# Optimization experiments

Hardware: AMD Instinct MI355X
Metric: run time of the kernel (lower is better)

Reference implementation:

```python
import jax, jax.numpy as jnp
import numpy as np
from jax import lax

B, C, FH, FW = 2, 128, 96, 160
H, W = 384, 640
NH, NP = 4, 9
T = 0.5


def conv(x, w, b, groups=1):
    pad = w.shape[2] // 2
    y = lax.conv_general_dilated(x, w, (1, 1), [(pad, pad), (pad, pad)],
                                 dimension_numbers=('NCHW', 'OIHW', 'NCHW'),
                                 feature_group_count=groups)
    return y + b[None, :, None, None]


def lrelu(x):
    return jnp.where(x >= 0, x, 0.1 * x)


def resize(x, h, w):
    # torch F.interpolate(mode='bilinear', align_corners=False, antialias=False)
    return jax.image.resize(x, (x.shape[0], x.shape[1], h, w), method='linear', antialias=False)


def grid_sample(vals, gx, gy, align_corners):
    # vals: (N, Ch, Hv, Wv); gx, gy: (N, Ho, Wo) normalized coords in [-1, 1]
    # bilinear, padding_mode='border'
    N, Ch, Hv, Wv = vals.shape
    if align_corners:
        x = (gx + 1.0) * 0.5 * (Wv - 1)
        y = (gy + 1.0) * 0.5 * (Hv - 1)
    else:
        x = ((gx + 1.0) * Wv - 1.0) * 0.5
        y = ((gy + 1.0) * Hv - 1.0) * 0.5
    x = jnp.clip(x, 0.0, Wv - 1.0)
    y = jnp.clip(y, 0.0, Hv - 1.0)
    x0 = jnp.floor(x)
    y0 = jnp.floor(y)
    wx = (x - x0)[:, None]  # (N,1,Ho,Wo)
    wy = (y - y0)[:, None]
    x0i = x0.astype(jnp.int32)
    y0i = y0.astype(jnp.int32)
    x1i = jnp.minimum(x0i + 1, Wv - 1)
    y1i = jnp.minimum(y0i + 1, Hv - 1)
    flat = vals.reshape(N, Ch, Hv * Wv)
    gather = jax.vmap(lambda v, i: jnp.take(v, i, axis=1))  # (Ch,HW),(Ho,Wo)->(Ch,Ho,Wo)
    v00 = gather(flat, y0i * Wv + x0i)
    v01 = gather(flat, y0i * Wv + x1i)
    v10 = gather(flat, y1i * Wv + x0i)
    v11 = gather(flat, y1i * Wv + x1i)
    return (v00 * (1 - wx) * (1 - wy) + v01 * wx * (1 - wy)
            + v10 * (1 - wx) * wy + v11 * wx * wy)


def warp(feat, flow):
    b, c, h, w = feat.shape
    if flow.shape[2:] != (h, w):
        sh, sw = h / flow.shape[2], w / flow.shape[3]
        flow = resize(flow, h, w) * jnp.array([sw, sh], flow.dtype)[None, :, None, None]
    gy, gx = jnp.meshgrid(jnp.arange(h, dtype=jnp.float32),
                          jnp.arange(w, dtype=jnp.float32), indexing='ij')
    gxn = 2.0 * (gx[None] + flow[:, 0]) / max(w - 1, 1) - 1.0
    gyn = 2.0 * (gy[None] + flow[:, 1]) / max(h - 1, 1) - 1.0
    return grid_sample(feat, gxn, gyn, True)


def group_norm(x, g, b, groups=8, eps=1e-5):
    B_, C_, h, w = x.shape
    xr = x.reshape(B_, groups, C_ // groups, h, w)
    m = xr.mean(axis=(2, 3, 4), keepdims=True)
    v = xr.var(axis=(2, 3, 4), keepdims=True)
    xn = ((xr - m) * lax.rsqrt(v + eps)).reshape(B_, C_, h, w)
    return xn * g[None, :, None, None] + b[None, :, None, None]


def deform_attn(q, src, ow0, ob0, ow1, ob1, aw0, ab0, aw1, ab1, vw, vb, pw, pb):
    b, c, h, w = q.shape
    hd = c // NH
    off = conv(lrelu(conv(q, ow0, ob0, groups=NH)), ow1, ob1).reshape(b, NH, NP, 2, h, w)
    attn = conv(lrelu(conv(q, aw0, ab0, groups=NH)), aw1, ab1).reshape(b, NH, NP, h, w)
    attn = jax.nn.softmax(attn, axis=2)
    vals = conv(src, vw, vb).reshape(b * NH, hd, h, w)
    gy, gx = jnp.meshgrid(jnp.arange(h, dtype=jnp.float32),
                          jnp.arange(w, dtype=jnp.float32), indexing='ij')
    sx = gx[None, None, None] + off[:, :, :, 0]  # (b,NH,NP,h,w)
    sy = gy[None, None, None] + off[:, :, :, 1]
    gxn = (2.0 * sx / max(w - 1, 1) - 1.0).reshape(b * NH, NP * h, w)
    gyn = (2.0 * sy / max(h - 1, 1) - 1.0).reshape(b * NH, NP * h, w)
    samp = grid_sample(vals, gxn, gyn, False).reshape(b, NH, hd, NP, h, w)
    out = (samp * attn[:, :, None]).sum(axis=3).reshape(b, c, h, w)
    return conv(out, pw, pb)


def setup_inputs() -> dict:
    key = jax.random.key(0)
    ks = jax.random.split(key, 24)
    rn = lambda k, s, sc: jax.random.normal(k, s, jnp.float32) * sc
    # offset conv bias: 3x3 regular grid init (n_points=9), padded with zeros
    gs = 3
    base = []
    for dy in range(gs):
        for dx in range(gs):
            base += [dx - gs // 2, dy - gs // 2]
    ob1 = np.zeros(NH * NP * 2, np.float32)
    ob1[:len(base)] = np.asarray(base, np.float32)
    return {
        'feat1': rn(ks[0], (B, C, FH, FW), 1.0),
        'feat2': rn(ks[1], (B, C, FH, FW), 1.0),
        'flow_fwd': rn(ks[2], (B, 2, H, W), 3.0),
        'flow_bwd': rn(ks[3], (B, 2, H, W), 3.0),
        'edge1': jax.random.uniform(ks[4], (B, 1, H, W), jnp.float32),
        'edge2': jax.random.uniform(ks[5], (B, 1, H, W), jnp.float32),
        'fuse_w0': rn(ks[6], (C, 2 * C + 3, 3, 3), 0.02),
        'fuse_b0': jnp.zeros((C,), jnp.float32),
        'fuse_w1': rn(ks[7], (C, C, 3, 3), 0.02),
        'fuse_b1': jnp.zeros((C,), jnp.float32),
        'gn_g': jnp.ones((C,), jnp.float32),
        'gn_b': jnp.zeros((C,), jnp.float32),
        'off_w0': rn(ks[8], (C, C // NH, 3, 3), 0.02),
        'off_b0': jnp.zeros((C,), jnp.float32),
        'off_w1': rn(ks[9], (NH * NP * 2, C, 1, 1), 0.01),
        'off_b1': jnp.asarray(ob1),
        'aw_w0': rn(ks[10], (C, C // NH, 3, 3), 0.02),
        'aw_b0': jnp.zeros((C,), jnp.float32),
        'aw_w1': rn(ks[11], (NH * NP, C, 1, 1), 0.02),
        'aw_b1': jnp.zeros((NH * NP,), jnp.float32),
        'val_w': rn(ks[12], (C, C, 1, 1), 0.05),
        'val_b': jnp.zeros((C,), jnp.float32),
        'out_w': rn(ks[13], (C, C, 1, 1), 0.05),
        'out_b': jnp.zeros((C,), jnp.float32),
        'ffn_w0': rn(ks[14], (2 * C, C, 1, 1), 0.05),
        'ffn_b0': jnp.zeros((2 * C,), jnp.float32),
        'ffn_w1': rn(ks[15], (C, 2 * C, 1, 1), 0.05),
        'ffn_b1': jnp.zeros((C,), jnp.float32),
        'dec_w0': rn(ks[16], (64, C, 3, 3), 0.03),
        'dec_b0': jnp.zeros((64,), jnp.float32),
        'dec_w1': rn(ks[17], (32, 64, 3, 3), 0.05),
        'dec_b1': jnp.zeros((32,), jnp.float32),
        'dec_w2': rn(ks[18], (3, 32, 3, 3), 0.05),
        'dec_b2': jnp.zeros((3,), jnp.float32),
    }


def reference(feat1, feat2, flow_fwd, flow_bwd, edge1, edge2,
              fuse_w0, fuse_b0, fuse_w1, fuse_b1, gn_g, gn_b,
              off_w0, off_b0, off_w1, off_b1, aw_w0, aw_b0, aw_w1, aw_b1,
              val_w, val_b, out_w, out_b, ffn_w0, ffn_b0, ffn_w1, ffn_b1,
              dec_w0, dec_b0, dec_w1, dec_b1, dec_w2, dec_b2):
    b, c, fh, fw = feat1.shape
    h, w = edge1.shape[2], edge1.shape[3]
    f1w = warp(feat1, flow_fwd * T)
    f2w = warp(feat2, flow_bwd * (1.0 - T))
    e1 = resize(edge1, fh, fw)
    e2 = resize(edge2, fh, fw)
    tmap = jnp.full((b, 1, fh, fw), T, feat1.dtype)
    fused = jnp.concatenate([f1w, f2w, e1, e2, tmap], axis=1)
    x = lrelu(conv(lrelu(conv(fused, fuse_w0, fuse_b0)), fuse_w1, fuse_b1))
    source = f1w * (1.0 - T) + f2w * T
    x = x + deform_attn(group_norm(x, gn_g, gn_b), source,
                        off_w0, off_b0, off_w1, off_b1,
                        aw_w0, aw_b0, aw_w1, aw_b1,
                        val_w, val_b, out_w, out_b)
    x = x + conv(jax.nn.gelu(conv(x, ffn_w0, ffn_b0), approximate=False), ffn_w1, ffn_b1)
    x = resize(x, h, w)
    x = lrelu(conv(x, dec_w0, dec_b0))
    x = lrelu(conv(x, dec_w1, dec_b1))
    return jax.nn.sigmoid(conv(x, dec_w2, dec_b2))
```

## Files before the change

kernel.cpp:

```cpp
#include <hip/hip_runtime.h>

typedef _Float16 f16;
typedef _Float16 f16x8 __attribute__((ext_vector_type(8)));
typedef float f32x4 __attribute__((ext_vector_type(4)));

constexpr int Bn = 2, Cn = 128, FH = 96, FW = 160, Hh = 384, Wh = 640;
constexpr int HWl = FH * FW;
constexpr int NHd = 4, NPt = 9;

#define DEVINL __device__ __forceinline__

DEVINL f32x4 zero4() { f32x4 z; z[0] = 0.f; z[1] = 0.f; z[2] = 0.f; z[3] = 0.f; return z; }
DEVINL f16x8 zero8() {
  f16x8 z;
#pragma unroll
  for (int j = 0; j < 8; ++j) z[j] = (f16)0.f;
  return z;
}

template<int ACT> DEVINL float activ(float v) {
  if (ACT == 1) return v >= 0.f ? v : 0.1f * v;
  if (ACT == 2) return 0.5f * v * (1.f + erff(v * 0.70710678118654752f));
  if (ACT == 3) return 1.f / (1.f + expf(-v));
  return v;
}

__global__ __launch_bounds__(256) void k_zero(f16* __restrict__ p, int n8)
{
  int i = blockIdx.x * 256 + threadIdx.x;
  if (i < n8) *(f16x8*)&p[(size_t)i * 8] = zero8();
}

struct PrepJob { const float* w; f16* wf; int Cout, cin_g, cout_g, KS, CoF, taps, CoFt, cf0, blk0; };
struct PrepArgs { PrepJob j[12]; };

__global__ __launch_bounds__(256) void k_wprep_all(PrepArgs a)
{
  int jb = 0;
#pragma unroll
  for (int t = 1; t < 12; ++t) if ((int)blockIdx.x >= a.j[t].blk0) jb = t;
  PrepJob J = a.j[jb];
  int idx = (blockIdx.x - J.blk0) * 256 + threadIdx.x;
  int total = J.taps * J.KS * J.CoF * 64;
  if (idx >= total) return;
  int lane = idx & 63;
  int rest = idx >> 6;
  int cf = rest % J.CoF;
  int rest2 = rest / J.CoF;
  int ks = rest2 % J.KS;
  int tap = rest2 / J.KS;
  int co = cf * 16 + (lane & 15);
  f16x8 v = zero8();
#pragma unroll
  for (int j = 0; j < 8; ++j) {
    int cip = ks * 32 + (lane >> 4) * 8 + j;
    int cil = cip - (co / J.cout_g) * J.cin_g;
    float x = 0.f;
    if (co < J.Cout && cil >= 0 && cil < J.cin_g)
      x = J.w[((size_t)co * J.cin_g + cil) * J.taps + tap];
    v[j] = (f16)x;
  }
  size_t oidx = (((size_t)tap * J.KS + ks) * J.CoFt + J.cf0 + cf) * 64 + lane;
  *(f16x8*)&J.wf[oidx * 8] = v;
}

__global__ __launch_bounds__(256) void k_tr_h(
    const float* __restrict__ feat1, const float* __restrict__ feat2,
    f16* __restrict__ t1, f16* __restrict__ t2)
{
  int idx = blockIdx.x * blockDim.x + threadIdx.x;
  if (idx >= 2 * Bn * HWl * 8) return;
  int cq = idx & 7;
  int pix = (idx >> 3) % HWl;
  int z = idx / (8 * HWl);
  int b = z & 1;
  const float* src = (z >> 1) ? feat2 : feat1;
  f16* dst = (z >> 1) ? t2 : t1;
  int c0 = cq * 16;
  f16x8 v0, v1;
#pragma unroll
  for (int j = 0; j < 8; ++j) {
    v0[j] = (f16)src[(size_t)(b * Cn + c0 + j) * HWl + pix];
    v1[j] = (f16)src[(size_t)(b * Cn + c0 + 8 + j) * HWl + pix];
  }
  f16* dp = dst + ((size_t)b * HWl + pix) * 128 + c0;
  *(f16x8*)dp = v0;
  *(f16x8*)(dp + 8) = v1;
}

__global__ __launch_bounds__(256) void k_warp_fuse_h(
    const f16* __restrict__ t1, const f16* __restrict__ t2,
    const float* __restrict__ flowf, const float* __restrict__ flowb,
    const float* __restrict__ edge1, const float* __restrict__ edge2,
    f16* __restrict__ fused, f16* __restrict__ src)
{
  int idx = blockIdx.x * blockDim.x + threadIdx.x;
  if (idx >= Bn * HWl * 8) return;
  int cq = idx & 7;
  int pix = (idx >> 3) % HWl;
  int b = idx / (8 * HWl);
  int j = pix % FW;
  int i = pix / FW;

  const int y4 = 4 * i + 1, x4 = 4 * j + 1;
  const float* p;
  p = flowf + (size_t)((b * 2 + 0) * Hh + y4) * Wh + x4;
  float fx1 = 0.03125f * (p[0] + p[1] + p[Wh] + p[Wh + 1]);
  p = flowf + (size_t)((b * 2 + 1) * Hh + y4) * Wh + x4;
  float fy1 = 0.03125f * (p[0] + p[1] + p[Wh] + p[Wh + 1]);
  p = flowb + (size_t)((b * 2 + 0) * Hh + y4) * Wh + x4;
  float fx2 = 0.03125f * (p[0] + p[1] + p[Wh] + p[Wh + 1]);
  p = flowb + (size_t)((b * 2 + 1) * Hh + y4) * Wh + x4;
  float fy2 = 0.03125f * (p[0] + p[1] + p[Wh] + p[Wh + 1]);

  float sx1 = fminf(fmaxf((float)j + fx1, 0.f), (float)(FW - 1));
  float sy1 = fminf(fmaxf((float)i + fy1, 0.f), (float)(FH - 1));
  float sx2 = fminf(fmaxf((float)j + fx2, 0.f), (float)(FW - 1));
  float sy2 = fminf(fmaxf((float)i + fy2, 0.f), (float)(FH - 1));

  int x10 = (int)floorf(sx1), y10 = (int)floorf(sy1);
  int x11 = min(x10 + 1, FW - 1), y11 = min(y10 + 1, FH - 1);
  float wx1 = sx1 - (float)x10, wy1 = sy1 - (float)y10;
  int x20 = (int)floorf(sx2), y20 = (int)floorf(sy2);
  int x21 = min(x20 + 1, FW - 1), y21 = min(y20 + 1, FH - 1);
  float wx2 = sx2 - (float)x20, wy2 = sy2 - (float)y20;

  float a00 = (1.f - wx1) * (1.f - wy1), a01 = wx1 * (1.f - wy1);
  float a10 = (1.f - wx1) * wy1,         a11 = wx1 * wy1;
  float c00 = (1.f - wx2) * (1.f - wy2), c01 = wx2 * (1.f - wy2);
  float c10 = (1.f - wx2) * wy2,         c11 = wx2 * wy2;

  int c0 = cq * 16;
  const f16* b1 = t1 + (size_t)b * HWl * 128 + c0;
  const f16* b2 = t2 + (size_t)b * HWl * 128 + c0;
  const f16x8* p100 = (const f16x8*)&b1[(size_t)(y10 * FW + x10) * 128];
  const f16x8* p101 = (const f16x8*)&b1[(size_t)(y10 * FW + x11) * 128];
  const f16x8* p110 = (const f16x8*)&b1[(size_t)(y11 * FW + x10) * 128];
  const f16x8* p111 = (const f16x8*)&b1[(size_t)(y11 * FW + x11) * 128];
  const f16x8* p200 = (const f16x8*)&b2[(size_t)(y20 * FW + x20) * 128];
  const f16x8* p201 = (const f16x8*)&b2[(size_t)(y20 * FW + x21) * 128];
  const f16x8* p210 = (const f16x8*)&b2[(size_t)(y21 * FW + x20) * 128];
  const f16x8* p211 = (const f16x8*)&b2[(size_t)(y21 * FW + x21) * 128];

  f16* fp = fused + ((size_t)b * HWl + pix) * 288;
  f16* sp = src + ((size_t)b * HWl + pix) * 128;

#pragma unroll
  for (int h = 0; h < 2; ++h) {
    f16x8 u00 = p100[h], u01 = p101[h], u10 = p110[h], u11 = p111[h];
    f16x8 w00 = p200[h], w01 = p201[h], w10 = p210[h], w11 = p211[h];
    f16x8 r1, r2, rs;
#pragma unroll
    for (int k = 0; k < 8; ++k) {
      float v1 = (float)u00[k] * a00 + (float)u01[k] * a01
               + (float)u10[k] * a10 + (float)u11[k] * a11;
      float v2 = (float)w00[k] * c00 + (float)w01[k] * c01
               + (float)w10[k] * c10 + (float)w11[k] * c11;
      r1[k] = (f16)v1; r2[k] = (f16)v2; rs[k] = (f16)(0.5f * (v1 + v2));
    }
    *(f16x8*)(fp + c0 + h * 8) = r1;
    *(f16x8*)(fp + 128 + c0 + h * 8) = r2;
    *(f16x8*)(sp + c0 + h * 8) = rs;
  }

  if (cq == 0) {
    p = edge1 + (size_t)(b * Hh + y4) * Wh + x4;
    float e1v = 0.25f * (p[0] + p[1] + p[Wh] + p[Wh + 1]);
    p = edge2 + (size_t)(b * Hh + y4) * Wh + x4;
    float e2v = 0.25f * (p[0] + p[1] + p[Wh] + p[Wh + 1]);
    fp[256] = (f16)e1v;
    fp[257] = (f16)e2v;
    fp[258] = (f16)0.5f;
#pragma unroll
    for (int c = 259; c < 288; ++c) fp[c] = (f16)0.f;
  }
}

template<int ACT, int M, int NF, int W, int KS>
__global__ __launch_bounds__(256, 2) void k_conv3g(
    const f16* __restrict__ X, const f16* __restrict__ Wf,
    const float* __restrict__ bias, const float* __restrict__ bias2, int bsplit,
    f16* __restrict__ Out, const f16* __restrict__ zpage,
    int CoF, int Cs_in, int Cs_out, int Htot,
    int in_r0, int in_rows, int out_r0, int out_rows,
    int ogr0, int nrows, int coTiles)
{
  int wid = blockIdx.x * 4 + (threadIdx.x >> 6);
  int lane = threadIdx.x & 63;
  int l15 = lane & 15, l4 = lane >> 4;
  int pixTiles = nrows * W / (M * 16);
  if (wid >= pixTiles * coTiles) return;
  int coT = wid % coTiles;
  int pixT = wid / coTiles;
  int b = blockIdx.z;
  int base = pixT * (M * 16);
  int row = ogr0 + base / W;
  int colB = base % W;

  f32x4 acc[M][NF];
#pragma unroll
  for (int mf = 0; mf < M; ++mf)
#pragma unroll
    for (int nf = 0; nf < NF; ++nf) acc[mf][nf] = zero4();

  const f16* rp[3];
#pragma unroll
  for (int ky = 0; ky < 3; ++ky) {
    int srow = row + ky - 1;
    bool rv = (srow >= 0 && srow < Htot);
    int crow = min(max(srow, in_r0), in_r0 + in_rows - 1);
    const f16* real = X + ((size_t)(b * in_rows + (crow - in_r0)) * W) * Cs_in + l4 * 8;
    rp[ky] = rv ? real : (zpage + l4 * 8);
  }
  int sc[3][M]; bool okc[3][M];
#pragma unroll
  for (int kx = 0; kx < 3; ++kx)
#pragma unroll
    for (int mf = 0; mf < M; ++mf) {
      int scol = colB + mf * 16 + l15 + kx - 1;
      okc[kx][mf] = (unsigned)scol < (unsigned)W;
      sc[kx][mf] = min(max(scol, 0), W - 1);
    }

  const f16* wb = Wf + (size_t)coT * NF * 512;
  constexpr int G = KS * 3;
  constexpr int NLD = 3 * (M + NF);
  constexpr int NMM = 3 * M * NF;

  f16x8 Afb[2][3][M];
  f16x8 Bfb[2][3][NF];

  auto loadGroup = [&](int g, int buf) {
    int cs = g / 3, ky = g % 3;
#pragma unroll
    for (int kx = 0; kx < 3; ++kx) {
#pragma unroll
      for (int mf = 0; mf < M; ++mf) {
        f16x8 t = *(const f16x8*)&rp[ky][(size_t)sc[kx][mf] * Cs_in + cs * 32];
        if ((kx == 0 && mf == 0) || (kx == 2 && mf == M - 1))
          t = okc[kx][mf] ? t : zero8();
        Afb[buf][kx][mf] = t;
      }
#pragma unroll
      for (int nf = 0; nf < NF; ++nf)
        Bfb[buf][kx][nf] =
            *(const f16x8*)&wb[((((size_t)(ky * 3 + kx) * KS + cs) * CoF + nf) * 64 + lane) * 8];
    }
  };

  loadGroup(0, 0);
  __builtin_amdgcn_sched_group_barrier(0x20, NLD, 0);
#pragma unroll
  for (int g = 0; g < G; ++g) {
    int cb = g & 1;
    if (g + 1 < G) loadGroup(g + 1, cb ^ 1);
#pragma unroll
    for (int kx = 0; kx < 3; ++kx)
#pragma unroll
      for (int mf = 0; mf < M; ++mf)
#pragma unroll
        for (int nf = 0; nf < NF; ++nf)
          acc[mf][nf] = __builtin_amdgcn_mfma_f32_16x16x32_f16(
              Afb[cb][kx][mf], Bfb[cb][kx][nf], acc[mf][nf], 0, 0, 0);
    if (g + 1 < G) __builtin_amdgcn_sched_group_barrier(0x20, NLD, 0);
    __builtin_amdgcn_sched_group_barrier(0x8, NMM, 0);
  }

  size_t rowoff = ((size_t)b * out_rows + (row - out_r0)) * W;
#pragma unroll
  for (int nf = 0; nf < NF; ++nf) {
    int co = coT * (NF * 16) + nf * 16 + l15;
    float bv = (co < bsplit) ? bias[co] : bias2[co - bsplit];
#pragma unroll
    for (int mf = 0; mf < M; ++mf) {
      int xo = colB + mf * 16 + l4 * 4;
#pragma unroll
      for (int rg = 0; rg < 4; ++rg) {
        float v = activ<ACT>(acc[mf][nf][rg] + bv);
        Out[(rowoff + xo + rg) * (size_t)Cs_out + co] = (f16)v;
      }
    }
  }
}

template<int ACT, int UP, int NF>
__global__ __launch_bounds__(256) void k_conv3m(
    const f16* __restrict__ Xin, const f16* __restrict__ Wf,
    const float* __restrict__ bias, f16* __restrict__ Out,
    int KS, int CoF, int Cs_in, int Cs_out, int Wd, int Ht,
    int in_r0, int in_rows, int out_r0, int out_rows, int ogr0, int ogr1)
{
  __shared__ f16 sA[8160];
  int tid = threadIdx.x;
  int wv = tid >> 6, lane = tid & 63;
  int l15 = lane & 15, l4 = lane >> 4;
  int colTiles = Wd >> 5;
  int tileC = blockIdx.x % colTiles, tileR = blockIdx.x / colTiles;
  int b = blockIdx.z;
  int co0 = blockIdx.y * (NF * 16);
  int cfB = blockIdx.y * NF;
  int rowBaseOut = ogr0 + tileR * 4;
  int rowBase = rowBaseOut - 1;
  int colBase = tileC * 32;

  f32x4 acc[2][NF];
#pragma unroll
  for (int mf = 0; mf < 2; ++mf)
#pragma unroll
    for (int nf = 0; nf < NF; ++nf) acc[mf][nf] = zero4();

  f16x8 stv[4];
  f16x8 stc[4][4];

  auto prefetch = [&](int cs) {
#pragma unroll
    for (int k = 0; k < 4; ++k) {
      int u = tid + k * 256;
      if (u < 816) {
        int s = u & 3;
        int pxy = u >> 2;
        int x = pxy % 34, y = pxy / 34;
        int gy = rowBase + y, gx = colBase + x - 1;
        if (UP) {
          stc[k][0] = zero8(); stc[k][1] = zero8();
          stc[k][2] = zero8(); stc[k][3] = zero8();
          if (gy >= 0 && gy < Ht && gx >= 0 && gx < Wd) {
            float uy = ((float)gy + 0.5f) * 0.25f - 0.5f;
            uy = fminf(fmaxf(uy, 0.f), (float)(FH - 1));
            int y0 = (int)floorf(uy);
            int y1 = min(y0 + 1, FH - 1);
            float ux = ((float)gx + 0.5f) * 0.25f - 0.5f;
            ux = fminf(fmaxf(ux, 0.f), (float)(FW - 1));
            int x0 = (int)floorf(ux);
            int x1 = min(x0 + 1, FW - 1);
            const f16* xb = Xin + (size_t)b * HWl * 128 + cs * 32 + s * 8;
            stc[k][0] = *(const f16x8*)&xb[(size_t)(y0 * FW + x0) * 128];
            stc[k][1] = *(const f16x8*)&xb[(size_t)(y0 * FW + x1) * 128];
            stc[k][2] = *(const f16x8*)&xb[(size_t)(y1 * FW + x0) * 128];
            stc[k][3] = *(const f16x8*)&xb[(size_t)(y1 * FW + x1) * 128];
          }
        } else {
          stv[k] = zero8();
          if (gy >= in_r0 && gy < in_r0 + in_rows && gx >= 0 && gx < Wd)
            stv[k] = *(const f16x8*)&Xin[(((size_t)b * in_rows + (gy - in_r0)) * Wd + gx) * Cs_in
                                         + cs * 32 + s * 8];
        }
      }
    }
  };

  auto writeLDS = [&]() {
#pragma unroll
    for (int k = 0; k < 4; ++k) {
      int u = tid + k * 256;
      if (u < 816) {
        int s = u & 3;
        int pxy = u >> 2;
        f16x8 v;
        if (UP) {
          int x = pxy % 34, y = pxy / 34;
          int gy = rowBase + y, gx = colBase + x - 1;
          float uy = ((float)gy + 0.5f) * 0.25f - 0.5f;
          uy = fminf(fmaxf(uy, 0.f), (float)(FH - 1));
          float fy = uy - floorf(uy);
          float ux = ((float)gx + 0.5f) * 0.25f - 0.5f;
          ux = fminf(fmaxf(ux, 0.f), (float)(FW - 1));
          float fx = ux - floorf(ux);
#pragma unroll
          for (int jj = 0; jj < 8; ++jj) {
            float t0 = (float)stc[k][0][jj] * (1.f - fx) + (float)stc[k][1][jj] * fx;
            float t1 = (float)stc[k][2][jj] * (1.f - fx) + (float)stc[k][3][jj] * fx;
            v[jj] = (f16)(t0 * (1.f - fy) + t1 * fy);
          }
        } else {
          v = stv[k];
        }
        *(f16x8*)((char*)sA + pxy * 80 + s * 16) = v;
      }
    }
  };

  prefetch(0);
  for (int cs = 0; cs < KS; ++cs) {
    writeLDS();
    __syncthreads();
    if (cs + 1 < KS) prefetch(cs + 1);
#pragma unroll
    for (int ky = 0; ky < 3; ++ky) {
#pragma unroll
      for (int kx = 0; kx < 3; ++kx) {
        const char* ab = (const char*)sA;
        f16x8 a0 = *(const f16x8*)(ab + ((wv + ky) * 34 + l15 + kx) * 80 + l4 * 16);
        f16x8 a1 = *(const f16x8*)(ab + ((wv + ky) * 34 + l15 + 16 + kx) * 80 + l4 * 16);
        int tap = ky * 3 + kx;
#pragma unroll
        for (int nf = 0; nf < NF; ++nf) {
          f16x8 bf = *(const f16x8*)&Wf[((((size_t)tap * KS + cs) * CoF + cfB + nf) * 64 + lane) * 8];
          acc[0][nf] = __builtin_amdgcn_mfma_f32_16x16x32_f16(a0, bf, acc[0][nf], 0, 0, 0);
          acc[1][nf] = __builtin_amdgcn_mfma_f32_16x16x32_f16(a1, bf, acc[1][nf], 0, 0, 0);
        }
      }
    }
    __syncthreads();
  }

  int r = rowBaseOut + wv;
  if (r < ogr1) {
    size_t rowoff = ((size_t)b * out_rows + (r - out_r0)) * Wd;
#pragma unroll
    for (int nf = 0; nf < NF; ++nf) {
      int co = co0 + nf * 16 + l15;
      float bv = bias[co];
#pragma unroll
      for (int mf = 0; mf < 2; ++mf) {
        int xo = colBase + mf * 16 + l4 * 4;
#pragma unroll
        for (int rg = 0; rg < 4; ++rg) {
          float v = activ<ACT>(acc[mf][nf][rg] + bv);
          Out[(rowoff + xo + rg) * Cs_out + co] = (f16)v;
        }
      }
    }
  }
}

template<int ACT, int RES, int KS>
__global__ __launch_bounds__(256, 2) void k_gemm1x1(
    const f16* __restrict__ X, const f16* __restrict__ Wf,
    const float* __restrict__ bias, f16* __restrict__ Out,
    int CoF, int Cs_in, int Cs_out, int Cr, int coTiles, int pixTiles)
{
  int wid = blockIdx.x * 4 + (threadIdx.x >> 6);
  int lane = threadIdx.x & 63;
  int total = pixTiles * coTiles;
  if (wid >= total) return;
  int coT = wid % coTiles;
  int pixT = wid / coTiles;
  int l15 = lane & 15, l4 = lane >> 4;

  f32x4 acc[2][4];
#pragma unroll
  for (int mf = 0; mf < 2; ++mf)
#pragma unroll
    for (int nf = 0; nf < 4; ++nf) acc[mf][nf] = zero4();

  int pA0 = pixT * 32 + l15;
  f16x8 Ab[2][2];
  f16x8 Bb[2][4];
  auto load = [&](int ks, int buf) {
    Ab[buf][0] = *(const f16x8*)&X[(size_t)pA0 * Cs_in + ks * 32 + l4 * 8];
    Ab[buf][1] = *(const f16x8*)&X[(size_t)(pA0 + 16) * Cs_in + ks * 32 + l4 * 8];
#pragma unroll
    for (int nf = 0; nf < 4; ++nf)
      Bb[buf][nf] = *(const f16x8*)&Wf[(((size_t)ks * CoF + coT * 4 + nf) * 64 + lane) * 8];
  };

  load(0, 0);
  __builtin_amdgcn_sched_group_barrier(0x20, 6, 0);
#pragma unroll
  for (int ks = 0; ks < KS; ++ks) {
    int cb = ks & 1;
    if (ks + 1 < KS) load(ks + 1, cb ^ 1);
#pragma unroll
    for (int nf = 0; nf < 4; ++nf) {
      acc[0][nf] = __builtin_amdgcn_mfma_f32_16x16x32_f16(Ab[cb][0], Bb[cb][nf], acc[0][nf], 0, 0, 0);
      acc[1][nf] = __builtin_amdgcn_mfma_f32_16x16x32_f16(Ab[cb][1], Bb[cb][nf], acc[1][nf], 0, 0, 0);
    }
    if (ks + 1 < KS) __builtin_amdgcn_sched_group_barrier(0x20, 6, 0);
    __builtin_amdgcn_sched_group_barrier(0x8, 8, 0);
  }
#pragma unroll
  for (int nf = 0; nf < 4; ++nf) {
    int co = coT * 64 + nf * 16 + l15;
    if (co < Cr) {
      float bv = bias[co];
#pragma unroll
      for (int mf = 0; mf < 2; ++mf) {
        int p0 = pixT * 32 + mf * 16 + l4 * 4;
#pragma unroll
        for (int rg = 0; rg < 4; ++rg) {
          float v = activ<ACT>(acc[mf][nf][rg] + bv);
          size_t o = (size_t)(p0 + rg) * Cs_out + co;
          if (RES) v += (float)Out[o];
          Out[o] = (f16)v;
        }
      }
    }
  }
}

__global__ __launch_bounds__(256) void k_gn_part_h(
    const f16* __restrict__ X, float* __restrict__ part)
{
  int s = blockIdx.x & 7;
  int g = (blockIdx.x >> 3) & 7;
  int b = blockIdx.x >> 6;
  int tid = threadIdx.x;
  const f16* Xp = X + (size_t)b * HWl * 128 + g * 16 + (tid & 1) * 8;
  float sum = 0.f, ss = 0.f;
  for (int p = s * 1920 + (tid >> 1); p < (s + 1) * 1920; p += 128) {
    f16x8 v = *(const f16x8*)&Xp[(size_t)p * 128];
#pragma unroll
    for (int jj = 0; jj < 8; ++jj) { float f = (float)v[jj]; sum += f; ss += f * f; }
  }
  __shared__ float sh1[256], sh2[256];
  sh1[tid] = sum; sh2[tid] = ss;
  __syncthreads();
  for (int st = 128; st > 0; st >>= 1) {
    if (tid < st) { sh1[tid] += sh1[tid + st]; sh2[tid] += sh2[tid + st]; }
    __syncthreads();
  }
  if (tid == 0) {
    part[((b * 8 + g) * 8 + s) * 2] = sh1[0];
    part[((b * 8 + g) * 8 + s) * 2 + 1] = sh2[0];
  }
}

__global__ __launch_bounds__(256) void k_gn_apply_h(
    const f16* __restrict__ X, const float* __restrict__ gw,
    const float* __restrict__ gb, const float* __restrict__ part,
    f16* __restrict__ Q)
{
  int idx = blockIdx.x * blockDim.x + threadIdx.x;
  int total = Bn * HWl * 16;
  if (idx >= total) return;
  int u = idx & 15;
  int pix = (idx >> 4) % HWl;
  int b = idx / (16 * HWl);
  int c0 = u * 8;
  int g = c0 >> 4;
  const float* pp = part + ((b * 8 + g) * 8) * 2;
  float sum = 0.f, ss = 0.f;
#pragma unroll
  for (int s = 0; s < 8; ++s) { sum += pp[s * 2]; ss += pp[s * 2 + 1]; }
  const float n = 16.f * HWl;
  float mean = sum / n;
  float var = ss / n - mean * mean;
  float inv = rsqrtf(var + 1e-5f);
  f16x8 v = *(const f16x8*)&X[((size_t)b * HWl + pix) * 128 + c0];
  f16x8 r;
#pragma unroll
  for (int jj = 0; jj < 8; ++jj) {
    int c = c0 + jj;
    r[jj] = (f16)(((float)v[jj] - mean) * (gw[c] * inv) + gb[c]);
  }
  *(f16x8*)&Q[((size_t)b * HWl + pix) * 128 + c0] = r;
}

__global__ __launch_bounds__(256) void k_softmax9_h(f16* __restrict__ a)
{
  int idx = blockIdx.x * blockDim.x + threadIdx.x;
  if (idx >= Bn * NHd * HWl) return;
  int pix = idx % HWl;
  int head = (idx / HWl) & 3;
  int b = idx / (HWl * NHd);
  f16* base = a + ((size_t)b * HWl + pix) * 48 + head * 9;
  float v[9];
  float m = -1e30f;
#pragma unroll
  for (int p0 = 0; p0 < 9; ++p0) { v[p0] = (float)base[p0]; m = fmaxf(m, v[p0]); }
  float s = 0.f;
#pragma unroll
  for (int p0 = 0; p0 < 9; ++p0) { v[p0] = expf(v[p0] - m); s += v[p0]; }
  float inv = 1.f / s;
#pragma unroll
  for (int p0 = 0; p0 < 9; ++p0) base[p0] = (f16)(v[p0] * inv);
}

__global__ __launch_bounds__(256) void k_deform_h(
    const f16* __restrict__ vals, const f16* __restrict__ off,
    const f16* __restrict__ attn, f16* __restrict__ outa)
{
  int idx = blockIdx.x * blockDim.x + threadIdx.x;
  if (idx >= Bn * NHd * HWl) return;
  int pix = idx % HWl;
  int head = (idx / HWl) & 3;
  int b = idx / (HWl * NHd);
  int j = pix % FW, i = pix / FW;

  const float kx = (float)FW / (float)(FW - 1);
  const float ky = (float)FH / (float)(FH - 1);
  const f16* vb = vals + (size_t)b * HWl * 128 + head * 32;
  const f16* ab = attn + ((size_t)b * HWl + pix) * 48 + head * 9;
  const f16* ob = off + ((size_t)b * HWl + pix) * 80 + head * 18;

  float acc[32];
#pragma unroll
  for (int k = 0; k < 32; ++k) acc[k] = 0.f;

#pragma unroll
  for (int p0 = 0; p0 < 9; ++p0) {
    float ox = (float)ob[p0 * 2];
    float oy = (float)ob[p0 * 2 + 1];
    float aw = (float)ab[p0];
    float xf = ((float)j + ox) * kx - 0.5f;
    float yf = ((float)i + oy) * ky - 0.5f;
    xf = fminf(fmaxf(xf, 0.f), (float)(FW - 1));
    yf = fminf(fmaxf(yf, 0.f), (float)(FH - 1));
    int x0 = (int)floorf(xf), y0 = (int)floorf(yf);
    int x1 = min(x0 + 1, FW - 1), y1 = min(y0 + 1, FH - 1);
    float fx = xf - (float)x0, fy = yf - (float)y0;
    float w00 = aw * (1.f - fx) * (1.f - fy);
    float w01 = aw * fx * (1.f - fy);
    float w10 = aw * (1.f - fx) * fy;
    float w11 = aw * fx * fy;
    const f16x8* c00 = (const f16x8*)&vb[(size_t)(y0 * FW + x0) * 128];
    const f16x8* c01 = (const f16x8*)&vb[(size_t)(y0 * FW + x1) * 128];
    const f16x8* c10 = (const f16x8*)&vb[(size_t)(y1 * FW + x0) * 128];
    const f16x8* c11 = (const f16x8*)&vb[(size_t)(y1 * FW + x1) * 128];
#pragma unroll
    for (int k8 = 0; k8 < 4; ++k8) {
      f16x8 a = c00[k8], bb = c01[k8], cc = c10[k8], dd = c11[k8];
#pragma unroll
      for (int jj = 0; jj < 8; ++jj)
        acc[k8 * 8 + jj] += w00 * (float)a[jj] + w01 * (float)bb[jj]
                          + w10 * (float)cc[jj] + w11 * (float)dd[jj];
    }
  }
  f16* op = outa + ((size_t)b * HWl + pix) * 128 + head * 32;
#pragma unroll
  for (int k = 0; k < 32; ++k) op[k] = (f16)acc[k];
}

__global__ __launch_bounds__(256) void k_dec2_h(
    const f16* __restrict__ Xb, const float* __restrict__ w,
    const float* __restrict__ bias, float* __restrict__ out,
    int c0, int b0, int brows, int R)
{
  int idx = blockIdx.x * blockDim.x + threadIdx.x;
  if (idx >= Bn * R * Wh) return;
  int x = idx % Wh;
  int y = c0 + (idx / Wh) % R;
  int b = idx / (Wh * R);
  float a0 = bias[0], a1 = bias[1], a2 = bias[2];
#pragma unroll
  for (int ky = 0; ky < 3; ++ky) {
    int gy = y + ky - 1;
    if (gy < 0 || gy >= Hh) continue;
#pragma unroll
    for (int kxx = 0; kxx < 3; ++kxx) {
      int gx = x + kxx - 1;
      if (gx < 0 || gx >= Wh) continue;
      int tap = ky * 3 + kxx;
      const f16* px = Xb + ((size_t)(b * brows + (gy - b0)) * Wh + gx) * 32;
#pragma unroll
      for (int k8 = 0; k8 < 4; ++k8) {
        f16x8 v = *(const f16x8*)&px[k8 * 8];
#pragma unroll
        for (int jj = 0; jj < 8; ++jj) {
          int ci = k8 * 8 + jj;
          float f = (float)v[jj];
          a0 += f * w[(0 * 32 + ci) * 9 + tap];
          a1 += f * w[(1 * 32 + ci) * 9 + tap];
          a2 += f * w[(2 * 32 + ci) * 9 + tap];
        }
      }
    }
  }
  size_t o = ((size_t)(b * 3 + 0) * Hh + y) * Wh + x;
  out[o] = 1.f / (1.f + expf(-a0));
  out[o + (size_t)Hh * Wh] = 1.f / (1.f + expf(-a1));
  out[o + (size_t)2 * Hh * Wh] = 1.f / (1.f + expf(-a2));
}

extern "C" void kernel_launch(void* const* d_in, const int* in_sizes, int n_in,
                              void* d_out, int out_size, void* d_ws, size_t ws_size,
                              hipStream_t stream) {
  (void)in_sizes; (void)n_in; (void)out_size; (void)ws_size;
  const float* feat1  = (const float*)d_in[0];
  const float* feat2  = (const float*)d_in[1];
  const float* flowf  = (const float*)d_in[2];
  const float* flowb  = (const float*)d_in[3];
  const float* edge1  = (const float*)d_in[4];
  const float* edge2  = (const float*)d_in[5];
  const float* fuse_w0 = (const float*)d_in[6];
  const float* fuse_b0 = (const float*)d_in[7];
  const float* fuse_w1 = (const float*)d_in[8];
  const float* fuse_b1 = (const float*)d_in[9];
  const float* gn_g   = (const float*)d_in[10];
  const float* gn_b   = (const float*)d_in[11];
  const float* off_w0 = (const float*)d_in[12];
  const float* off_b0 = (const float*)d_in[13];
  const float* off_w1 = (const float*)d_in[14];
  const float* off_b1 = (const float*)d_in[15];
  const float* aw_w0  = (const float*)d_in[16];
  const float* aw_b0  = (const float*)d_in[17];
  const float* aw_w1  = (const float*)d_in[18];
  const float* aw_b1  = (const float*)d_in[19];
  const float* val_w  = (const float*)d_in[20];
  const float* val_b  = (const float*)d_in[21];
  const float* out_w  = (const float*)d_in[22];
  const float* out_b  = (const float*)d_in[23];
  const float* ffn_w0 = (const float*)d_in[24];
  const float* ffn_b0 = (const float*)d_in[25];
  const float* ffn_w1 = (const float*)d_in[26];
  const float* ffn_b1 = (const float*)d_in[27];
  const float* dec_w0 = (const float*)d_in[28];
  const float* dec_b0 = (const float*)d_in[29];
  const float* dec_w1 = (const float*)d_in[30];
  const float* dec_b1 = (const float*)d_in[31];
  const float* dec_w2 = (const float*)d_in[32];
  const float* dec_b2 = (const float*)d_in[33];
  float* out = (float*)d_out;

  f16* ws16 = (f16*)d_ws;
  size_t o = 0;
  auto alloc = [&](size_t n) { f16* p = ws16 + o; o += (n + 7) & ~(size_t)7; return p; };
  f16* xbuf  = alloc((size_t)2 * HWl * 128);
  f16* zp    = alloc(98304);
  f16* wfF0 = alloc(9 * 9 * 8 * 512);
  f16* wfF1 = alloc(9 * 4 * 8 * 512);
  f16* wfOA = alloc(9 * 4 * 16 * 512);
  f16* wfD0 = alloc(9 * 4 * 4 * 512);
  f16* wfD1 = alloc(9 * 2 * 2 * 512);
  f16* w1O  = alloc(4 * 5 * 512);
  f16* w1A  = alloc(4 * 3 * 512);
  f16* w1V  = alloc(4 * 8 * 512);
  f16* w1U  = alloc(4 * 8 * 512);
  f16* w1G0 = alloc(4 * 16 * 512);
  f16* w1G1 = alloc(8 * 8 * 512);
  float* gnp = (float*)alloc(512);
  f16* pool  = ws16 + o;
  f16* regA  = alloc((size_t)2 * HWl * 288);
  f16* regB  = alloc((size_t)2 * HWl * 128);
  f16* regC  = alloc((size_t)2 * HWl * 128);
  f16* offb  = alloc((size_t)2 * HWl * 80);
  f16* attnb = alloc((size_t)2 * HWl * 48);
  f16* regF  = alloc((size_t)2 * HWl * 131);
  f16* featT1 = alloc((size_t)2 * HWl * 128);
  f16* featT2 = alloc((size_t)2 * HWl * 128);

  f16* fused = regA;
  f16* t_oa  = regA;
  f16* ffn_t = regA;
  f16* src_h = regB;
  f16* out_attn = regB;
  f16* tmp_h = regC;
  f16* qb    = regC;
  f16* valsb = regF;
  f16* bufA = pool;
  f16* bufB = bufA + (size_t)2 * 196 * 640 * 64;

  dim3 blk(256);
  auto pg = [](long n) { return dim3((unsigned)((n + 255) / 256)); };
  auto cg = [](int pixTiles, int coTiles) {
    return dim3((unsigned)((pixTiles * coTiles + 3) / 4), 1, 2);
  };
  const int BIG = 1 << 30;

  k_zero<<<dim3(48), blk, 0, stream>>>(zp, 12288);

  PrepArgs pa;
  int pb = 0;
  auto addj = [&](int k, const float* w, f16* wf, int Cout, int cing, int coutg,
                  int KS, int CoF, int taps, int CoFt, int cf0) {
    pa.j[k] = PrepJob{w, wf, Cout, cing, coutg, KS, CoF, taps, CoFt, cf0, pb};
    pb += (taps * KS * CoF * 64 + 255) / 256;
  };
  addj(0, fuse_w0, wfF0, 128, 259, 128, 9, 8, 9, 8, 0);
  addj(1, fuse_w1, wfF1, 128, 128, 128, 4, 8, 9, 8, 0);
  addj(2, off_w0, wfOA, 128, 32, 32, 4, 8, 9, 16, 0);
  addj(3, aw_w0,  wfOA, 128, 32, 32, 4, 8, 9, 16, 8);
  addj(4, dec_w0, wfD0, 64, 128, 64, 4, 4, 9, 4, 0);
  addj(5, dec_w1, wfD1, 32, 64, 32, 2, 2, 9, 2, 0);
  addj(6, off_w1, w1O, 72, 128, 72, 4, 5, 1, 5, 0);
  addj(7, aw_w1,  w1A, 36, 128, 36, 4, 3, 1, 3, 0);
  addj(8, val_w,  w1V, 128, 128, 128, 4, 8, 1, 8, 0);
  addj(9, out_w,  w1U, 128, 128, 128, 4, 8, 1, 8, 0);
  addj(10, ffn_w0, w1G0, 256, 128, 256, 4, 16, 1, 16, 0);
  addj(11, ffn_w1, w1G1, 128, 256, 128, 8, 8, 1, 8, 0);
  k_wprep_all<<<dim3((unsigned)pb), blk, 0, stream>>>(pa);

  k_tr_h<<<pg(2L * Bn * HWl * 8), blk, 0, stream>>>(feat1, feat2, featT1, featT2);
  k_warp_fuse_h<<<pg((long)Bn * HWl * 8), blk, 0, stream>>>(featT1, featT2, flowf, flowb,
                                                            edge1, edge2, fused, src_h);
  k_conv3g<1, 2, 4, 160, 9><<<cg(480, 2), blk, 0, stream>>>(fused, wfF0, fuse_b0, fuse_b0, BIG,
      tmp_h, zp, 8, 288, 128, FH, 0, FH, 0, FH, 0, FH, 2);
  k_conv3g<1, 2, 4, 160, 4><<<cg(480, 2), blk, 0, stream>>>(tmp_h, wfF1, fuse_b1, fuse_b1, BIG,
      xbuf, zp, 8, 128, 128, FH, 0, FH, 0, FH, 0, FH, 2);
  k_gn_part_h<<<dim3(128), blk, 0, stream>>>(xbuf, gnp);
  k_gn_apply_h<<<pg(2L * HWl * 16), blk, 0, stream>>>(xbuf, gn_g, gn_b, gnp, qb);
  k_conv3g<1, 2, 4, 160, 4><<<cg(480, 4), blk, 0, stream>>>(qb, wfOA, off_b0, aw_b0, 128,
      t_oa, zp, 16, 128, 256, FH, 0, FH, 0, FH, 0, FH, 4);
  k_gemm1x1<0, 0, 4><<<dim3(480), blk, 0, stream>>>(t_oa, w1O, off_b1, offb,
      5, 256, 80, 72, 2, 960);
  k_gemm1x1<0, 0, 4><<<dim3(240), blk, 0, stream>>>(t_oa + 128, w1A, aw_b1, attnb,
      3, 256, 48, 36, 1, 960);
  k_softmax9_h<<<pg(2L * NHd * HWl), blk, 0, stream>>>(attnb);
  k_gemm1x1<0, 0, 4><<<dim3(480), blk, 0, stream>>>(src_h, w1V, val_b, valsb,
      8, 128, 128, 128, 2, 960);
  k_deform_h<<<pg(2L * NHd * HWl), blk, 0, stream>>>(valsb, offb, attnb, out_attn);
  k_gemm1x1<0, 1, 4><<<dim3(480), blk, 0, stream>>>(out_attn, w1U, out_b, xbuf,
      8, 128, 128, 128, 2, 960);
  k_gemm1x1<2, 0, 4><<<dim3(960), blk, 0, stream>>>(xbuf, w1G0, ffn_b0, ffn_t,
      16, 128, 256, 256, 4, 960);
  k_gemm1x1<0, 1, 8><<<dim3(480), blk, 0, stream>>>(ffn_t, w1G1, ffn_b1, xbuf,
      8, 256, 128, 128, 2, 960);

  for (int c0 = 0; c0 < Hh; c0 += 192) {
    int c1 = c0 + 192;
    int a0 = c0 - 2 > 0 ? c0 - 2 : 0;
    int a1 = c1 + 2 < Hh ? c1 + 2 : Hh;
    int b0 = c0 - 1 > 0 ? c0 - 1 : 0;
    int b1 = c1 + 1 < Hh ? c1 + 1 : Hh;
    int ar = a1 - a0, br = b1 - b0;
    dim3 gD0((unsigned)(((ar + 3) / 4) * 20), 1, 2);
    k_conv3m<1, 1, 4><<<gD0, blk, 0, stream>>>(xbuf, wfD0, dec_b0, bufA,
        4, 4, 128, 64, Wh, Hh, 0, 0, a0, ar, a0, a1);
    dim3 gD1((unsigned)(((br + 3) / 4) * 20), 1, 2);
    k_conv3m<1, 0, 2><<<gD1, blk, 0, stream>>>(bufA, wfD1, dec_b1, bufB,
        2, 2, 64, 32, Wh, Hh, a0, ar, b0, br, b0, b1);
    k_dec2_h<<<pg(2L * 192 * Wh), blk, 0, stream>>>(bufB, dec_w2, dec_b2, out,
                                                    c0, b0, br, 192);
  }
}
```

Baseline: 519.2 us.

## Materialize upsampled decoder input per chunk instead of fusing bilinear resize into conv

```diff
diff --git a/kernel.cpp b/kernel.cpp
--- a/kernel.cpp
+++ b/kernel.cpp
@@ -421,6 +421,48 @@
         }
       }
     }
+  }
+}
+
+__global__ __launch_bounds__(256) void k_up4_h(
+    const f16* __restrict__ Xl, f16* __restrict__ U, int u0, int urows)
+{
+  int idx = blockIdx.x * blockDim.x + threadIdx.x;
+  if (idx >= Bn * urows * Wh * 8) return;
+  int cq = idx & 7;
+  int x = (idx >> 3) % Wh;
+  int r = ((idx >> 3) / Wh) % urows;
+  int b = idx / (8 * Wh * urows);
+  int R = u0 + r;
+
+  float uy = ((float)R + 0.5f) * 0.25f - 0.5f;
+  uy = fminf(fmaxf(uy, 0.f), (float)(FH - 1));
+  int y0 = (int)floorf(uy);
+  int y1 = min(y0 + 1, FH - 1);
+  float fy = uy - (float)y0;
+  float ux = ((float)x + 0.5f) * 0.25f - 0.5f;
+  ux = fminf(fmaxf(ux, 0.f), (float)(FW - 1));
+  int x0 = (int)floorf(ux);
+  int x1 = min(x0 + 1, FW - 1);
+  float fx = ux - (float)x0;
+
+  const f16* xb = Xl + (size_t)b * HWl * 128 + cq * 16;
+  const f16x8* c00 = (const f16x8*)&xb[(size_t)(y0 * FW + x0) * 128];
+  const f16x8* c01 = (const f16x8*)&xb[(size_t)(y0 * FW + x1) * 128];
+  const f16x8* c10 = (const f16x8*)&xb[(size_t)(y1 * FW + x0) * 128];
+  const f16x8* c11 = (const f16x8*)&xb[(size_t)(y1 * FW + x1) * 128];
+  f16* up = U + (((size_t)b * urows + r) * Wh + x) * 128 + cq * 16;
+#pragma unroll
+  for (int h = 0; h < 2; ++h) {
+    f16x8 a = c00[h], bb = c01[h], cc = c10[h], dd = c11[h];
+    f16x8 o;
+#pragma unroll
+    for (int jj = 0; jj < 8; ++jj) {
+      float t0 = (float)a[jj] * (1.f - fx) + (float)bb[jj] * fx;
+      float t1 = (float)cc[jj] * (1.f - fx) + (float)dd[jj] * fx;
+      o[jj] = (f16)(t0 * (1.f - fy) + t1 * fy);
+    }
+    *(f16x8*)(up + h * 8) = o;
   }
 }
 
@@ -738,8 +780,9 @@
   f16* tmp_h = regC;
   f16* qb    = regC;
   f16* valsb = regF;
-  f16* bufA = pool;
-  f16* bufB = bufA + (size_t)2 * 196 * 640 * 64;
+  f16* bufU = pool;
+  f16* bufA = bufU + (size_t)2 * 103 * 640 * 128;
+  f16* bufB = bufA + (size_t)2 * 100 * 640 * 64;
 
   dim3 blk(256);
   auto pg = [](long n) { return dim3((unsigned)((n + 255) / 256)); };
@@ -797,20 +840,23 @@
   k_gemm1x1<0, 1, 8><<<dim3(480), blk, 0, stream>>>(ffn_t, w1G1, ffn_b1, xbuf,
       8, 256, 128, 128, 2, 960);
 
-  for (int c0 = 0; c0 < Hh; c0 += 192) {
-    int c1 = c0 + 192;
+  for (int c0 = 0; c0 < Hh; c0 += 96) {
+    int c1 = c0 + 96;
     int a0 = c0 - 2 > 0 ? c0 - 2 : 0;
     int a1 = c1 + 2 < Hh ? c1 + 2 : Hh;
     int b0 = c0 - 1 > 0 ? c0 - 1 : 0;
     int b1 = c1 + 1 < Hh ? c1 + 1 : Hh;
-    int ar = a1 - a0, br = b1 - b0;
+    int u0 = a0 - 1 > 0 ? a0 - 1 : 0;
+    int u1 = a1 + 1 < Hh ? a1 + 1 : Hh;
+    int ar = a1 - a0, br = b1 - b0, ur = u1 - u0;
+    k_up4_h<<<pg(2L * ur * Wh * 8), blk, 0, stream>>>(xbuf, bufU, u0, ur);
     dim3 gD0((unsigned)(((ar + 3) / 4) * 20), 1, 2);
-    k_conv3m<1, 1, 4><<<gD0, blk, 0, stream>>>(xbuf, wfD0, dec_b0, bufA,
-        4, 4, 128, 64, Wh, Hh, 0, 0, a0, ar, a0, a1);
+    k_conv3m<1, 0, 4><<<gD0, blk, 0, stream>>>(bufU, wfD0, dec_b0, bufA,
+        4, 4, 128, 64, Wh, Hh, u0, ur, a0, ar, a0, a1);
     dim3 gD1((unsigned)(((br + 3) / 4) * 20), 1, 2);
     k_conv3m<1, 0, 2><<<gD1, blk, 0, stream>>>(bufA, wfD1, dec_b1, bufB,
         2, 2, 64, 32, Wh, Hh, a0, ar, b0, br, b0, b1);
-    k_dec2_h<<<pg(2L * 192 * Wh), blk, 0, stream>>>(bufB, dec_w2, dec_b2, out,
-                                                    c0, b0, br, 192);
-  }
-}
+    k_dec2_h<<<pg(2L * 96 * Wh), blk, 0, stream>>>(bufB, dec_w2, dec_b2, out,
+                                                   c0, b0, br, 96);
+  }
+}
```

Result: slower. 618.5 us (+19.1%).
